# Optimization experiments

Hardware: AMD Instinct MI355X
Metric: run time of the kernel (lower is better)

## Reference

```python
import jax, jax.numpy as jnp
import numpy as np

N_NODES = 100000

def setup_inputs() -> dict:
    key = jax.random.key(0)
    ks = jax.random.split(key, 8)
    n_feat, nhid, nclass = 256, 128, 40
    n_edges = 1600000
    x = jax.random.normal(ks[0], (N_NODES, n_feat), dtype=jnp.float32)
    edge_index = jax.random.randint(ks[1], (2, n_edges), 0, N_NODES, dtype=jnp.int64)
    # Glorot-ish scaled weights
    W1 = jax.random.normal(ks[2], (n_feat, nhid), dtype=jnp.float32) / np.sqrt(n_feat)
    b1 = jnp.zeros((nhid,), dtype=jnp.float32)
    W2 = jax.random.normal(ks[3], (nhid, nhid), dtype=jnp.float32) / np.sqrt(nhid)
    b2 = jnp.zeros((nhid,), dtype=jnp.float32)
    Wc = jax.random.normal(ks[4], (nhid, nclass), dtype=jnp.float32) / np.sqrt(nhid)
    bc = jnp.zeros((nclass,), dtype=jnp.float32)
    return {"x": x, "edge_index": edge_index, "W1": W1, "b1": b1,
            "W2": W2, "b2": b2, "Wc": Wc, "bc": bc}


def _gcn_conv(x, src, dst, W, b, n_nodes):
    """PyG GCNConv: transform, then sym-normalized aggregation with self-loops.
    out_i = sum_{j in N(i) u {i}} (d_i^-1/2 d_j^-1/2) (x_j W) + b,
    where d = in-degree over A + I.
    """
    h = x @ W  # [N, out]
    ones = jnp.ones_like(dst, dtype=h.dtype)
    deg = jax.ops.segment_sum(ones, dst, num_segments=n_nodes) + 1.0  # + self loop
    dinv = jax.lax.rsqrt(deg)  # deg >= 1, always valid
    norm = dinv[src] * dinv[dst]  # [E]
    msg = h[src] * norm[:, None]  # [E, out]  (dominant gather traffic)
    agg = jax.ops.segment_sum(msg, dst, num_segments=n_nodes)
    agg = agg + h * (dinv * dinv)[:, None]  # self-loop contribution
    return agg + b


def reference(x, edge_index, W1, b1, W2, b2, Wc, bc):
    # eval mode: dropout is identity
    src, dst = edge_index[0], edge_index[1]
    n = x.shape[0]
    h = jax.nn.relu(_gcn_conv(x, src, dst, W1, b1, n))
    h = jax.nn.relu(_gcn_conv(h, src, dst, W2, b2, n))
    return h @ Wc + bc
```

## Files before the change

kernel.cpp:

```cpp
#include <hip/hip_runtime.h>
#include <hip/hip_bf16.h>
#include <hip/hip_fp16.h>
#include <type_traits>


typedef _Float16 half8 __attribute__((ext_vector_type(8)));
typedef _Float16 half4v __attribute__((ext_vector_type(4)));
typedef float floatx4 __attribute__((ext_vector_type(4)));

#define EPB 8192


__device__ inline int block_incl_scan_256(int t, int* tmp) {
    int tid = threadIdx.x;
    tmp[tid] = t;
    __syncthreads();
    #pragma unroll
    for (int off = 1; off < 256; off <<= 1) {
        int v = (tid >= off) ? tmp[tid - off] : 0;
        __syncthreads();
        tmp[tid] += v;
        __syncthreads();
    }
    return tmp[tid];
}

template <int ITEMS>
__global__ __launch_bounds__(256) void k_scan1(const int* __restrict__ v,
                                               int* __restrict__ bsum, int n) {
    __shared__ int tmp[256];
    int base = blockIdx.x * (256 * ITEMS) + threadIdx.x * ITEMS;
    int t = 0;
    #pragma unroll
    for (int l = 0; l < ITEMS; ++l) {
        int i = base + l;
        t += (i < n) ? v[i] : 0;
    }
    block_incl_scan_256(t, tmp);
    if (threadIdx.x == 0) bsum[blockIdx.x] = tmp[255];
}

__global__ __launch_bounds__(256) void k_scan2(int* __restrict__ bsum, int nb) {
    __shared__ int tmp[256];
    int tid = threadIdx.x;
    int v = (tid < nb) ? bsum[tid] : 0;
    block_incl_scan_256(v, tmp);
    if (tid < nb) bsum[tid] = tid ? tmp[tid - 1] : 0;
}

template <int ITEMS>
__global__ __launch_bounds__(256) void k_scan3(const int* __restrict__ vin,
                                               const int* __restrict__ bsum,
                                               int* __restrict__ rp, int n) {
    __shared__ int tmp[256];
    int base = blockIdx.x * (256 * ITEMS) + threadIdx.x * ITEMS;
    int v[ITEMS];
    int t = 0;
    #pragma unroll
    for (int l = 0; l < ITEMS; ++l) {
        int i = base + l;
        v[l] = (i < n) ? vin[i] : 0;
        t += v[l];
    }
    block_incl_scan_256(t, tmp);
    int run = bsum[blockIdx.x] + (threadIdx.x ? tmp[threadIdx.x - 1] : 0);
    #pragma unroll
    for (int l = 0; l < ITEMS; ++l) {
        int i = base + l;
        if (i < n) rp[i] = run;
        run += v[l];
    }
}


__global__ __launch_bounds__(256) void k_histA(const int* __restrict__ dst,
                                               int* __restrict__ histM,
                                               int E, int nblk) {
    __shared__ int h[512];
    int tid = threadIdx.x;
    for (int i = tid; i < 512; i += 256) h[i] = 0;
    __syncthreads();
    int base = blockIdx.x * EPB;
    #pragma unroll 4
    for (int l = 0; l < EPB / 256; ++l) {
        int i = base + l * 256 + tid;
        if (i < E) atomicAdd(&h[dst[i] >> 8], 1);
    }
    __syncthreads();
    for (int i = tid; i < 512; i += 256)
        histM[i * nblk + blockIdx.x] = h[i];
}

__global__ __launch_bounds__(256) void k_scatterA(const int* __restrict__ src,
                                                  const int* __restrict__ dst,
                                                  const int* __restrict__ histS,
                                                  unsigned long long* __restrict__ eB,
                                                  int E, int nblk) {
    __shared__ int bse[512];
    __shared__ int cnt[512];
    int tid = threadIdx.x;
    for (int i = tid; i < 512; i += 256) {
        bse[i] = histS[i * nblk + blockIdx.x];
        cnt[i] = 0;
    }
    __syncthreads();
    int base = blockIdx.x * EPB;
    #pragma unroll 4
    for (int l = 0; l < EPB / 256; ++l) {
        int i = base + l * 256 + tid;
        if (i < E) {
            int d = dst[i];
            int s = src[i];
            int b = d >> 8;
            int r = atomicAdd(&cnt[b], 1);
            eB[bse[b] + r] = ((unsigned long long)(unsigned)d << 32) | (unsigned)s;
        }
    }
}

#define BCAP 4608
__global__ __launch_bounds__(256) void k_sortB(const unsigned long long* __restrict__ eB,
                                               const int* __restrict__ histS,
                                               int* __restrict__ srcS,
                                               int* __restrict__ rowptr,
                                               float* __restrict__ dinv,
                                               int n, int E, int nblk) {
    const int b   = blockIdx.x;
    const int tid = threadIdx.x;
    const int ni0 = b << 8;
    int s0 = histS[b * nblk];
    int s1 = (b < 511) ? histS[(b + 1) * nblk] : E;
    int cnt = s1 - s0;
    if (cnt > BCAP) cnt = BCAP;
    if (cnt == 0 && ni0 > n) return;

    __shared__ int hist[256];
    __shared__ int tmp[256];
    __shared__ int baseA[256];
    __shared__ int cntA[256];
    __shared__ int dstL[BCAP];
    __shared__ unsigned srcL[BCAP];
    __shared__ int lbA[256];

    hist[tid] = 0;
    cntA[tid] = 0;
    __syncthreads();
    for (int i = s0 + tid; i < s0 + cnt; i += 256) {
        int d = (int)(eB[i] >> 32);
        atomicAdd(&hist[d & 255], 1);
    }
    __syncthreads();
    int own  = hist[tid];
    int incl = block_incl_scan_256(own, tmp);
    baseA[tid] = incl - own;
    __syncthreads();
    for (int i = s0 + tid; i < s0 + cnt; i += 256) {
        unsigned long long v = eB[i];
        int d = (int)(v >> 32);
        int dig = d & 255;
        int r = atomicAdd(&cntA[dig], 1);
        int pos = baseA[dig] + r;
        dstL[pos] = d;
        srcL[pos] = (unsigned)v;
    }
    __syncthreads();
    for (int j = tid; j < cnt; j += 256)
        srcS[s0 + j] = (int)srcL[j];
    if (ni0 <= n) {
        int i = ni0 + tid;
        int lo = 0, hi = cnt;
        while (lo < hi) {
            int mid = (lo + hi) >> 1;
            if (dstL[mid] < i) lo = mid + 1; else hi = mid;
        }
        lbA[tid] = lo;
        __syncthreads();
        if (i <= n) {
            rowptr[i] = s0 + lo;
            if (i < n) {
                int ub = (tid < 255) ? lbA[tid + 1] : cnt;
                dinv[i] = rsqrtf((float)(ub - lo + 1));
            }
        }
    }
}

__global__ __launch_bounds__(256) void k_wcast_all(const float* __restrict__ W1,
                                                   _Float16* __restrict__ W1t,
                                                   const float* __restrict__ W2,
                                                   _Float16* __restrict__ W2t,
                                                   const float* __restrict__ Wc,
                                                   _Float16* __restrict__ Wct) {
    int i = blockIdx.x * 256 + threadIdx.x;
    if (i < 32768) {
        int c = i >> 8, k = i & 255;
        W1t[i] = (_Float16)W1[(size_t)k * 128 + c];
    } else if (i < 32768 + 16384) {
        int j = i - 32768;
        int c = j >> 7, k = j & 127;
        W2t[j] = (_Float16)W2[(size_t)k * 128 + c];
    } else if (i < 32768 + 16384 + 6144) {
        int j = i - 32768 - 16384;
        int c = j >> 7, k = j & 127;
        Wct[j] = (c < 40) ? (_Float16)Wc[(size_t)k * 40 + c] : (_Float16)0.f;
    }
}


template <int K, int BN, int MT, typename AT, typename OT>
__global__ __launch_bounds__(256) void gemm_bres(const AT* __restrict__ A,
                                                 const _Float16* __restrict__ Wt,
                                                 const float* __restrict__ bias,
                                                 OT* __restrict__ C,
                                                 int M, int N) {
    constexpr int KC = (K > 128) ? 128 : K;
    constexpr int KP = KC + 8;
    constexpr int NT = BN / 16;
    __shared__ __align__(16) _Float16 Bs[BN * KP];

    const int tid  = threadIdx.x;
    const int lane = tid & 63;
    const int wv   = tid >> 6;
    const int qd   = lane >> 4;
    const int ln15 = lane & 15;
    const int bm   = blockIdx.x * (64 * MT);

    floatx4 acc[MT][NT];
    #pragma unroll
    for (int mt = 0; mt < MT; ++mt)
        #pragma unroll
        for (int c = 0; c < NT; ++c) acc[mt][c] = (floatx4){0.f, 0.f, 0.f, 0.f};

    int rw[MT];
    #pragma unroll
    for (int mt = 0; mt < MT; ++mt) {
        int r = bm + (wv * MT + mt) * 16 + ln15;
        rw[mt] = (r < M) ? r : (M - 1);
    }

    #pragma unroll
    for (int kh = 0; kh < K; kh += KC) {
        constexpr int TOT = BN * KC / 8;
        for (int i = tid; i < TOT; i += 256) {
            int idx = i * 8;
            int col = idx / KC;
            int kk  = idx % KC;
            *(uint4*)&Bs[col * KP + kk] =
                *(const uint4*)(Wt + (size_t)col * K + kh + kk);
        }
        __syncthreads();

        #pragma unroll
        for (int ks = 0; ks < KC / 32; ++ks) {
            const int k0 = kh + ks * 32;
            half8 a[MT];
            #pragma unroll
            for (int mt = 0; mt < MT; ++mt) {
                if constexpr (std::is_same<AT, float>::value) {
                    const float* p = A + (size_t)rw[mt] * K + k0 + qd * 8;
                    float4 v0 = *(const float4*)p;
                    float4 v1 = *(const float4*)(p + 4);
                    half8 h;
                    h[0] = (_Float16)v0.x; h[1] = (_Float16)v0.y;
                    h[2] = (_Float16)v0.z; h[3] = (_Float16)v0.w;
                    h[4] = (_Float16)v1.x; h[5] = (_Float16)v1.y;
                    h[6] = (_Float16)v1.z; h[7] = (_Float16)v1.w;
                    a[mt] = h;
                } else {
                    a[mt] = *(const half8*)((const _Float16*)A +
                                            (size_t)rw[mt] * K + k0 + qd * 8);
                }
            }
            #pragma unroll
            for (int c = 0; c < NT; ++c) {
                half8 b = *(const half8*)&Bs[(c * 16 + ln15) * KP + ks * 32 + qd * 8];
                #pragma unroll
                for (int mt = 0; mt < MT; ++mt)
                    acc[mt][c] = __builtin_amdgcn_mfma_f32_16x16x32_f16(a[mt], b,
                                                                        acc[mt][c], 0, 0, 0);
            }
        }
        __syncthreads();
    }

    #pragma unroll
    for (int mt = 0; mt < MT; ++mt) {
        int baseRow = bm + (wv * MT + mt) * 16 + qd * 4;
        #pragma unroll
        for (int c = 0; c < NT; ++c) {
            int col = c * 16 + ln15;
            if constexpr (std::is_same<OT, _Float16>::value) {
                #pragma unroll
                for (int r = 0; r < 4; ++r) {
                    int row = baseRow + r;
                    if (row < M) C[(size_t)row * N + col] = (_Float16)acc[mt][c][r];
                }
            } else {
                float bv = (col < N && bias) ? bias[col] : 0.f;
                #pragma unroll
                for (int r = 0; r < 4; ++r) {
                    int row = baseRow + r;
                    if (row < M && col < N)
                        ((float*)C)[(size_t)row * N + col] = acc[mt][c][r] + bv;
                }
            }
        }
    }
}


static __device__ __forceinline__ float2 h2f2u(unsigned int raw) {
    __half2 h = *(__half2*)&raw;
    return __half22float2(h);
}

__global__ __launch_bounds__(256) void gcn_agg(const unsigned int* __restrict__ h,
                                               const int* __restrict__ rowptr,
                                               const int* __restrict__ srcS,
                                               const float* __restrict__ dinv,
                                               const float* __restrict__ bias,
                                               unsigned int* __restrict__ out,
                                               int n, int do_relu) {
    int node = blockIdx.x * 4 + (threadIdx.x >> 6);
    if (node >= n) return;
    const int lane = threadIdx.x & 63;
    const int g    = lane >> 4;
    const int t    = lane & 15;

    const _Float16* hb = (const _Float16*)h;

    float di = dinv[node];
    int e0 = rowptr[node];
    int e1 = rowptr[node + 1];

    half8 sv = *(const half8*)(hb + (size_t)(unsigned)node * 128 + t * 8);
    const float4* b4 = (const float4*)bias;
    float4 blo = b4[t * 2 + 0];
    float4 bhi = b4[t * 2 + 1];

    float2 acc[4];
    #pragma unroll
    for (int i = 0; i < 4; ++i) acc[i] = make_float2(0.f, 0.f);

    for (int ce = e0; ce < e1; ce += 64) {
        int cnt = e1 - ce;
        cnt = (cnt < 64) ? cnt : 64;
        int colv = 0, wval = 0;
        if (lane < cnt) {
            int c = srcS[ce + lane];
            colv = c;
            wval = __float_as_int(di * dinv[c]);
        }
        #pragma unroll 2
        for (int d = 0; d < cnt; d += 4) {
            int idx = (d + g) << 2;
            int c   = __builtin_amdgcn_ds_bpermute(idx, colv);
            float w = __int_as_float(__builtin_amdgcn_ds_bpermute(idx, wval));
            const unsigned* hp = (const unsigned*)(hb + (size_t)(unsigned)c * 128 + t * 8);
            uint4 hv = *(const uint4*)hp;
            float2 u0 = h2f2u(hv.x);
            float2 u1 = h2f2u(hv.y);
            float2 u2 = h2f2u(hv.z);
            float2 u3 = h2f2u(hv.w);
            acc[0].x += u0.x * w; acc[0].y += u0.y * w;
            acc[1].x += u1.x * w; acc[1].y += u1.y * w;
            acc[2].x += u2.x * w; acc[2].y += u2.y * w;
            acc[3].x += u3.x * w; acc[3].y += u3.y * w;
        }
    }

    #pragma unroll
    for (int i = 0; i < 4; ++i) {
        acc[i].x += __shfl_xor(acc[i].x, 16);
        acc[i].y += __shfl_xor(acc[i].y, 16);
        acc[i].x += __shfl_xor(acc[i].x, 32);
        acc[i].y += __shfl_xor(acc[i].y, 32);
    }

    float s = di * di;
    float bb[8] = {blo.x, blo.y, blo.z, blo.w, bhi.x, bhi.y, bhi.z, bhi.w};
    half8 o;
    #pragma unroll
    for (int i = 0; i < 8; ++i) {
        float v = ((i & 1) ? acc[i >> 1].y : acc[i >> 1].x) + (float)sv[i] * s + bb[i];
        if (do_relu) v = fmaxf(v, 0.f);
        o[i] = (_Float16)v;
    }
    if (g == 0)
        *(half8*)((_Float16*)out + (size_t)(unsigned)node * 128 + t * 8) = o;
}


extern "C" void kernel_launch(void* const* d_in, const int* in_sizes, int n_in,
                              void* d_out, int out_size, void* d_ws, size_t ws_size,
                              hipStream_t stream) {
    const float* x  = (const float*)d_in[0];
    const int* eidx = (const int*)d_in[1];
    const float* W1 = (const float*)d_in[2];
    const float* b1 = (const float*)d_in[3];
    const float* W2 = (const float*)d_in[4];
    const float* b2 = (const float*)d_in[5];
    const float* Wc = (const float*)d_in[6];
    const float* bc = (const float*)d_in[7];
    float* out = (float*)d_out;

    const int NF = 256, NH = 128, NC = 40;
    const int n = in_sizes[0] / NF;
    const int E = in_sizes[1] / 2;
    const int* src = eidx;
    const int* dst = eidx + E;

    const int nblk = (E + EPB - 1) / EPB;
    const int hm   = 512 * nblk;
    const int nbA  = (hm + 4095) / 4096;

    char* wsb = (char*)d_ws;
    size_t off = 0;
    auto alloc = [&](size_t bytes) {
        char* p = wsb + off;
        off = (off + bytes + 511) & ~(size_t)511;
        return p;
    };
    _Float16* hbuf = (_Float16*)alloc((size_t)n * NH * 2);
    _Float16* abuf = (_Float16*)alloc((size_t)n * NH * 2);
    _Float16* W1t  = (_Float16*)alloc((size_t)128 * 256 * 2);
    _Float16* W2t  = (_Float16*)alloc((size_t)128 * 128 * 2);
    _Float16* Wct  = (_Float16*)alloc((size_t)48 * 128 * 2);
    unsigned long long* eB = (unsigned long long*)alloc((size_t)E * 8);
    int* srcS      = (int*)alloc((size_t)E * 4);
    int* histM     = (int*)alloc((size_t)hm * 4);
    int* histS     = (int*)alloc((size_t)hm * 4);
    int* rowptr    = (int*)alloc((size_t)(n + 1) * 4);
    float* dinv    = (float*)alloc((size_t)n * 4);
    int* bsumA     = (int*)alloc(1024);

    k_histA<<<nblk, 256, 0, stream>>>(dst, histM, E, nblk);
    k_scan1<16><<<nbA, 256, 0, stream>>>(histM, bsumA, hm);
    k_scan2<<<1, 256, 0, stream>>>(bsumA, nbA);
    k_scan3<16><<<nbA, 256, 0, stream>>>(histM, bsumA, histS, hm);
    k_scatterA<<<nblk, 256, 0, stream>>>(src, dst, histS, eB, E, nblk);
    k_sortB<<<512, 256, 0, stream>>>(eB, histS, srcS, rowptr, dinv, n, E, nblk);

    k_wcast_all<<<(32768 + 16384 + 6144 + 255) / 256, 256, 0, stream>>>(
        W1, W1t, W2, W2t, Wc, Wct);

    const int gB = (n + 127) / 128;
    gemm_bres<256, 128, 2, float, _Float16><<<gB, 256, 0, stream>>>(x, W1t, nullptr, hbuf, n, NH);
    gcn_agg<<<(n + 3) / 4, 256, 0, stream>>>((const unsigned int*)hbuf, rowptr, srcS, dinv, b1,
                                             (unsigned int*)abuf, n, 1);
    gemm_bres<128, 128, 2, _Float16, _Float16><<<gB, 256, 0, stream>>>(abuf, W2t, nullptr, hbuf, n, NH);
    gcn_agg<<<(n + 3) / 4, 256, 0, stream>>>((const unsigned int*)hbuf, rowptr, srcS, dinv, b2,
                                             (unsigned int*)abuf, n, 1);
    gemm_bres<128, 48, 2, _Float16, float><<<gB, 256, 0, stream>>>(abuf, Wct, bc, out, n, NC);
}
```

Baseline: 413.8 us.

## Prefetch A rows into registers before staging weights, one M-tile per wave

Replaces the GEMM kernel with a variant that issues every A-row load for the whole K range into registers before staging the weight tile in shared memory. The global A latency can then overlap with the weight copy and the barrier. Each wave now handles a single 16-row tile, so blocks cover 64 rows and the grid doubles. The full K extent of the weights now sits in LDS at once. For K=256 that is about 67KB per block, which can limit occupancy, and weight staging is repeated across twice as many blocks.

Result: faster. 394.8 us (-4.6%).

```diff
diff --git a/kernel.cpp b/kernel.cpp
--- a/kernel.cpp
+++ b/kernel.cpp
@@ -5,7 +5,6 @@
 
 
 typedef _Float16 half8 __attribute__((ext_vector_type(8)));
-typedef _Float16 half4v __attribute__((ext_vector_type(4)));
 typedef float floatx4 __attribute__((ext_vector_type(4)));
 
 #define EPB 8192
@@ -207,15 +206,15 @@
 }
 
 
-template <int K, int BN, int MT, typename AT, typename OT>
-__global__ __launch_bounds__(256) void gemm_bres(const AT* __restrict__ A,
-                                                 const _Float16* __restrict__ Wt,
-                                                 const float* __restrict__ bias,
-                                                 OT* __restrict__ C,
-                                                 int M, int N) {
-    constexpr int KC = (K > 128) ? 128 : K;
-    constexpr int KP = KC + 8;
+template <int K, int BN, typename AT, typename OT>
+__global__ __launch_bounds__(256) void gemm_pf(const AT* __restrict__ A,
+                                               const _Float16* __restrict__ Wt,
+                                               const float* __restrict__ bias,
+                                               OT* __restrict__ C,
+                                               int M, int N) {
+    constexpr int KP = K + 8;
     constexpr int NT = BN / 16;
+    constexpr int KS = K / 32;
     __shared__ __align__(16) _Float16 Bs[BN * KP];
 
     const int tid  = threadIdx.x;
@@ -223,86 +222,78 @@
     const int wv   = tid >> 6;
     const int qd   = lane >> 4;
     const int ln15 = lane & 15;
-    const int bm   = blockIdx.x * (64 * MT);
-
-    floatx4 acc[MT][NT];
-    #pragma unroll
-    for (int mt = 0; mt < MT; ++mt)
+    const int bm   = blockIdx.x * 64;
+
+    int row  = bm + wv * 16 + ln15;
+    int rowc = (row < M) ? row : (M - 1);
+
+    float4 af[std::is_same<AT, float>::value ? KS : 1][2];
+    half8  ah[std::is_same<AT, float>::value ? 1 : KS];
+    if constexpr (std::is_same<AT, float>::value) {
+        const float* p = A + (size_t)rowc * K + qd * 8;
         #pragma unroll
-        for (int c = 0; c < NT; ++c) acc[mt][c] = (floatx4){0.f, 0.f, 0.f, 0.f};
-
-    int rw[MT];
-    #pragma unroll
-    for (int mt = 0; mt < MT; ++mt) {
-        int r = bm + (wv * MT + mt) * 16 + ln15;
-        rw[mt] = (r < M) ? r : (M - 1);
-    }
-
-    #pragma unroll
-    for (int kh = 0; kh < K; kh += KC) {
-        constexpr int TOT = BN * KC / 8;
-        for (int i = tid; i < TOT; i += 256) {
-            int idx = i * 8;
-            int col = idx / KC;
-            int kk  = idx % KC;
-            *(uint4*)&Bs[col * KP + kk] =
-                *(const uint4*)(Wt + (size_t)col * K + kh + kk);
-        }
-        __syncthreads();
-
+        for (int ks = 0; ks < KS; ++ks) {
+            af[ks][0] = *(const float4*)(p + ks * 32);
+            af[ks][1] = *(const float4*)(p + ks * 32 + 4);
+        }
+    } else {
+        const _Float16* p = (const _Float16*)A + (size_t)rowc * K + qd * 8;
         #pragma unroll
-        for (int ks = 0; ks < KC / 32; ++ks) {
-            const int k0 = kh + ks * 32;
-            half8 a[MT];
-            #pragma unroll
-            for (int mt = 0; mt < MT; ++mt) {
-                if constexpr (std::is_same<AT, float>::value) {
-                    const float* p = A + (size_t)rw[mt] * K + k0 + qd * 8;
-                    float4 v0 = *(const float4*)p;
-                    float4 v1 = *(const float4*)(p + 4);
-                    half8 h;
-                    h[0] = (_Float16)v0.x; h[1] = (_Float16)v0.y;
-                    h[2] = (_Float16)v0.z; h[3] = (_Float16)v0.w;
-                    h[4] = (_Float16)v1.x; h[5] = (_Float16)v1.y;
-                    h[6] = (_Float16)v1.z; h[7] = (_Float16)v1.w;
-                    a[mt] = h;
-                } else {
-                    a[mt] = *(const half8*)((const _Float16*)A +
-                                            (size_t)rw[mt] * K + k0 + qd * 8);
-                }
-            }
-            #pragma unroll
-            for (int c = 0; c < NT; ++c) {
-                half8 b = *(const half8*)&Bs[(c * 16 + ln15) * KP + ks * 32 + qd * 8];
-                #pragma unroll
-                for (int mt = 0; mt < MT; ++mt)
-                    acc[mt][c] = __builtin_amdgcn_mfma_f32_16x16x32_f16(a[mt], b,
-                                                                        acc[mt][c], 0, 0, 0);
-            }
-        }
-        __syncthreads();
-    }
-
-    #pragma unroll
-    for (int mt = 0; mt < MT; ++mt) {
-        int baseRow = bm + (wv * MT + mt) * 16 + qd * 4;
+        for (int ks = 0; ks < KS; ++ks)
+            ah[ks] = *(const half8*)(p + ks * 32);
+    }
+
+    constexpr int TOT = BN * K / 8;
+    #pragma unroll
+    for (int i = 0; i < TOT / 256; ++i) {
+        int idx = (i * 256 + tid) * 8;
+        int col = idx / K;
+        int kk  = idx % K;
+        *(uint4*)&Bs[col * KP + kk] = *(const uint4*)(Wt + idx);
+    }
+    __syncthreads();
+
+    floatx4 acc[NT];
+    #pragma unroll
+    for (int c = 0; c < NT; ++c) acc[c] = (floatx4){0.f, 0.f, 0.f, 0.f};
+
+    #pragma unroll
+    for (int ks = 0; ks < KS; ++ks) {
+        half8 a;
+        if constexpr (std::is_same<AT, float>::value) {
+            float4 v0 = af[ks][0];
+            float4 v1 = af[ks][1];
+            a[0] = (_Float16)v0.x; a[1] = (_Float16)v0.y;
+            a[2] = (_Float16)v0.z; a[3] = (_Float16)v0.w;
+            a[4] = (_Float16)v1.x; a[5] = (_Float16)v1.y;
+            a[6] = (_Float16)v1.z; a[7] = (_Float16)v1.w;
+        } else {
+            a = ah[ks];
+        }
         #pragma unroll
         for (int c = 0; c < NT; ++c) {
-            int col = c * 16 + ln15;
-            if constexpr (std::is_same<OT, _Float16>::value) {
-                #pragma unroll
-                for (int r = 0; r < 4; ++r) {
-                    int row = baseRow + r;
-                    if (row < M) C[(size_t)row * N + col] = (_Float16)acc[mt][c][r];
-                }
-            } else {
-                float bv = (col < N && bias) ? bias[col] : 0.f;
-                #pragma unroll
-                for (int r = 0; r < 4; ++r) {
-                    int row = baseRow + r;
-                    if (row < M && col < N)
-                        ((float*)C)[(size_t)row * N + col] = acc[mt][c][r] + bv;
-                }
+            half8 b = *(const half8*)&Bs[(c * 16 + ln15) * KP + ks * 32 + qd * 8];
+            acc[c] = __builtin_amdgcn_mfma_f32_16x16x32_f16(a, b, acc[c], 0, 0, 0);
+        }
+    }
+
+    int baseRow = bm + wv * 16 + qd * 4;
+    #pragma unroll
+    for (int c = 0; c < NT; ++c) {
+        int col = c * 16 + ln15;
+        if constexpr (std::is_same<OT, _Float16>::value) {
+            #pragma unroll
+            for (int r = 0; r < 4; ++r) {
+                int rr = baseRow + r;
+                if (rr < M) C[(size_t)rr * N + col] = (_Float16)acc[c][r];
+            }
+        } else {
+            float bv = (col < N && bias) ? bias[col] : 0.f;
+            #pragma unroll
+            for (int r = 0; r < 4; ++r) {
+                int rr = baseRow + r;
+                if (rr < M && col < N)
+                    ((float*)C)[(size_t)rr * N + col] = acc[c][r] + bv;
             }
         }
     }
@@ -444,12 +435,12 @@
     k_wcast_all<<<(32768 + 16384 + 6144 + 255) / 256, 256, 0, stream>>>(
         W1, W1t, W2, W2t, Wc, Wct);
 
-    const int gB = (n + 127) / 128;
-    gemm_bres<256, 128, 2, float, _Float16><<<gB, 256, 0, stream>>>(x, W1t, nullptr, hbuf, n, NH);
+    const int gB = (n + 63) / 64;
+    gemm_pf<256, 128, float, _Float16><<<gB, 256, 0, stream>>>(x, W1t, nullptr, hbuf, n, NH);
     gcn_agg<<<(n + 3) / 4, 256, 0, stream>>>((const unsigned int*)hbuf, rowptr, srcS, dinv, b1,
                                              (unsigned int*)abuf, n, 1);
-    gemm_bres<128, 128, 2, _Float16, _Float16><<<gB, 256, 0, stream>>>(abuf, W2t, nullptr, hbuf, n, NH);
+    gemm_pf<128, 128, _Float16, _Float16><<<gB, 256, 0, stream>>>(abuf, W2t, nullptr, hbuf, n, NH);
     gcn_agg<<<(n + 3) / 4, 256, 0, stream>>>((const unsigned int*)hbuf, rowptr, srcS, dinv, b2,
                                              (unsigned int*)abuf, n, 1);
-    gemm_bres<128, 48, 2, _Float16, float><<<gB, 256, 0, stream>>>(abuf, Wct, bc, out, n, NC);
-}
+    gemm_pf<128, 48, _Float16, float><<<gB, 256, 0, stream>>>(abuf, Wct, bc, out, n, NC);
+}
```
